# Kernel optimization log

Hardware: AMD Instinct MI355X
Metric: run time of the kernel (lower is better)

The kernel has to match this reference:

```python
import jax, jax.numpy as jnp
import numpy as np

D_MODEL, D_FF, N_EXPERTS, TOP_K = 1024, 4096, 8, 2
B, S = 4, 2048


def setup_inputs() -> dict:
    key = jax.random.key(0)
    ks = jax.random.split(key, 6)
    scale_in = 1.0 / np.sqrt(D_MODEL)
    scale_ff = 1.0 / np.sqrt(D_FF)
    return {
        "x": jax.random.normal(ks[0], (B, S, D_MODEL), jnp.float32),
        "gate_w": jax.random.normal(ks[1], (N_EXPERTS, D_MODEL), jnp.float32) * 0.01,
        "w1": jax.random.normal(ks[2], (N_EXPERTS, D_MODEL, D_FF), jnp.float32) * scale_in,
        "b1": jax.random.normal(ks[3], (N_EXPERTS, D_FF), jnp.float32) * 0.01,
        "w2": jax.random.normal(ks[4], (N_EXPERTS, D_FF, D_MODEL), jnp.float32) * scale_ff,
        "b2": jax.random.normal(ks[5], (N_EXPERTS, D_MODEL), jnp.float32) * 0.01,
    }


def reference(x, gate_w, w1, b1, w2, b2):
    # x: [B, S, D]; gate_w: [E, D]; w1: [E, D, F]; w2: [E, F, D]
    Bb, Ss, D = x.shape
    E = gate_w.shape[0]
    logits = jnp.einsum("bsd,ed->bse", x, gate_w)
    probs = jax.nn.softmax(logits, axis=-1)
    top_p, top_i = jax.lax.top_k(probs, TOP_K)                # [B,S,K]
    top_p = top_p / (jnp.sum(top_p, axis=-1, keepdims=True) + 1e-9)
    T = Bb * Ss
    x_flat = x.reshape(T, D)
    idx = top_i.reshape(T, TOP_K)
    val = top_p.reshape(T, TOP_K)
    # per-token combine weight for each expert: [T, E]
    comb = jnp.zeros((T, E), x.dtype).at[jnp.arange(T)[:, None], idx].add(val)
    out = jnp.zeros_like(x_flat)
    for e in range(E):  # small fixed expert count
        h = jax.nn.gelu(x_flat @ w1[e] + b1[e], approximate=False)
        y = h @ w2[e] + b2[e]
        out = out + y * comb[:, e:e + 1]
    return out.reshape(Bb, Ss, D)
```

## Files before the change

kernel.cpp:

```cpp
#include <hip/hip_runtime.h>
#include <hip/hip_bf16.h>
#include <cstdint>

#define D_MODEL 1024
#define D_FF    4096
#define NEXP    8
#define TOPK    2
#define TOKENS  8192
#define NPAIR   (TOKENS * TOPK)
#define NPAD    (NPAIR + 128)

typedef __bf16 bf16x8 __attribute__((ext_vector_type(8)));
typedef float  f32x4  __attribute__((ext_vector_type(4)));

__device__ __forceinline__ unsigned short f2bf(float f) {
    unsigned int u = __float_as_uint(f);
    unsigned int r = (u + 0x7FFFu + ((u >> 16) & 1u)) >> 16;
    return (unsigned short)r;
}

__device__ __forceinline__ void lds_load16(void* lds, const void* g) {
    __builtin_amdgcn_global_load_lds(
        (const __attribute__((address_space(1))) void*)g,
        (__attribute__((address_space(3))) void*)lds, 16, 0, 0);
}

__device__ __forceinline__ float fast_gelu(float v) {
    float y2 = 1.5957691216f * (v + 0.044715f * v * v * v);
    float t = 1.0f - 2.0f / (__expf(y2) + 1.0f);
    return 0.5f * v * (1.0f + t);
}

__global__ __launch_bounds__(64) void gate_kernel(
        const float* __restrict__ x, const float* __restrict__ gw,
        int* __restrict__ tok_e, float* __restrict__ tok_w)
{
    const int t = blockIdx.x;
    const int lane = threadIdx.x;
    const float* xr = x + (size_t)t * D_MODEL;
    float xv[16];
#pragma unroll
    for (int i = 0; i < 16; ++i) xv[i] = xr[lane + 64 * i];
    float lg[NEXP];
#pragma unroll
    for (int e = 0; e < NEXP; ++e) {
        const float* g = gw + e * D_MODEL;
        float s = 0.f;
#pragma unroll
        for (int i = 0; i < 16; ++i) s += xv[i] * g[lane + 64 * i];
        for (int off = 32; off; off >>= 1) s += __shfl_down(s, off);
        lg[e] = s;
    }
    if (lane == 0) {
        float m = lg[0];
#pragma unroll
        for (int e = 1; e < NEXP; ++e) m = fmaxf(m, lg[e]);
        float ex[NEXP], S = 0.f;
#pragma unroll
        for (int e = 0; e < NEXP; ++e) { ex[e] = expf(lg[e] - m); S += ex[e]; }
        int i0 = 0; float p0 = ex[0];
#pragma unroll
        for (int e = 1; e < NEXP; ++e) if (ex[e] > p0) { p0 = ex[e]; i0 = e; }
        int i1 = -1; float p1 = -1.f;
#pragma unroll
        for (int e = 0; e < NEXP; ++e) if (e != i0 && ex[e] > p1) { p1 = ex[e]; i1 = e; }
        float q0 = p0 / S, q1 = p1 / S;
        float denom = q0 + q1 + 1e-9f;
        tok_e[2 * t] = i0; tok_e[2 * t + 1] = i1;
        tok_w[2 * t] = q0 / denom; tok_w[2 * t + 1] = q1 / denom;
    }
}

__global__ __launch_bounds__(256) void count_kernel(
        const int* __restrict__ tok_e, int* __restrict__ cnt)
{
    __shared__ int lc[NEXP];
    const int t = blockIdx.x * 256 + threadIdx.x;
    if (threadIdx.x < NEXP) lc[threadIdx.x] = 0;
    __syncthreads();
    atomicAdd(&lc[tok_e[2 * t]], 1);
    atomicAdd(&lc[tok_e[2 * t + 1]], 1);
    __syncthreads();
    if (threadIdx.x < NEXP) atomicAdd(&cnt[threadIdx.x], lc[threadIdx.x]);
}

__global__ void offsets_kernel(const int* __restrict__ cnt, int* __restrict__ offs,
                               int* __restrict__ fill)
{
    if (threadIdx.x == 0 && blockIdx.x == 0) {
        int s = 0;
        for (int e = 0; e < NEXP; ++e) { offs[e] = s; fill[e] = s; s += cnt[e]; }
        offs[NEXP] = s;
    }
}

__global__ __launch_bounds__(256) void scatter2_kernel(
        const int* __restrict__ tok_e, const float* __restrict__ tok_w,
        int* __restrict__ fill, int* __restrict__ pair_tok, float* __restrict__ pair_w)
{
    __shared__ int lc[NEXP], lbase[NEXP];
    const int t = blockIdx.x * 256 + threadIdx.x;
    if (threadIdx.x < NEXP) lc[threadIdx.x] = 0;
    __syncthreads();
    const int e0 = tok_e[2 * t], e1 = tok_e[2 * t + 1];
    const int r0 = atomicAdd(&lc[e0], 1);
    const int r1 = atomicAdd(&lc[e1], 1);
    __syncthreads();
    if (threadIdx.x < NEXP)
        lbase[threadIdx.x] = atomicAdd(&fill[threadIdx.x], lc[threadIdx.x]);
    __syncthreads();
    const int p0 = lbase[e0] + r0, p1 = lbase[e1] + r1;
    pair_tok[p0] = t; pair_w[p0] = tok_w[2 * t];
    pair_tok[p1] = t; pair_w[p1] = tok_w[2 * t + 1];
}

__global__ __launch_bounds__(256) void gather_cvt(
        const float* __restrict__ x, const int* __restrict__ pair_tok,
        unsigned short* __restrict__ Xg)
{
    int p = blockIdx.x;
    int tok = pair_tok[p];
    const float4* src = (const float4*)(x + (size_t)tok * D_MODEL);
    ushort4* dst = (ushort4*)(Xg + (size_t)p * D_MODEL);
    float4 v = src[threadIdx.x];
    ushort4 o;
    o.x = f2bf(v.x); o.y = f2bf(v.y); o.z = f2bf(v.z); o.w = f2bf(v.w);
    dst[threadIdx.x] = o;
}

__global__ __launch_bounds__(256) void transpose_cvt(
        const float* __restrict__ in, unsigned short* __restrict__ out, int R, int C)
{
    __shared__ float tile[32][33];
    const int e = blockIdx.z;
    const int r0 = blockIdx.y * 32, c0 = blockIdx.x * 32;
    const float* src = in + (size_t)e * R * C;
    unsigned short* dst = out + (size_t)e * R * C;
    const int tx = threadIdx.x & 31, ty = threadIdx.x >> 5;
#pragma unroll
    for (int i = 0; i < 32; i += 8)
        tile[ty + i][tx] = src[(size_t)(r0 + ty + i) * C + (c0 + tx)];
    __syncthreads();
#pragma unroll
    for (int i = 0; i < 32; i += 8)
        dst[(size_t)(c0 + ty + i) * R + (r0 + tx)] = f2bf(tile[tx][ty + i]);
}

#define MOE_STAGE3(PA, PB, K0, LD) \
    lds_load16(PA + t * 8,        ag + (K0)); \
    lds_load16(PA + 2048 + t * 8, ag + (size_t)64 * (LD) + (K0)); \
    lds_load16(PB + t * 8,        bg + (K0)); \
    lds_load16(PB + 2048 + t * 8, bg + (size_t)64 * (LD) + (K0));

#define MOE_COMPUTE3(PA, PB) { \
    bf16x8 a_[4], b_[4]; \
    _Pragma("unroll") \
    for (int i_ = 0; i_ < 4; ++i_) { \
        a_[i_] = *(const bf16x8*)&PA[(wm * 64 + i_ * 16 + lm) * 32 + qs8]; \
        b_[i_] = *(const bf16x8*)&PB[(wn * 64 + i_ * 16 + lm) * 32 + qs8]; \
    } \
    __builtin_amdgcn_s_setprio(1); \
    _Pragma("unroll") \
    for (int i_ = 0; i_ < 4; ++i_) \
    _Pragma("unroll") \
    for (int j_ = 0; j_ < 4; ++j_) \
        c[i_][j_] = __builtin_amdgcn_mfma_f32_16x16x32_bf16(a_[i_], b_[j_], c[i_][j_], 0, 0, 0); \
    __builtin_amdgcn_s_setprio(0); }

#define MOE_KLOOP(KTOT, LD) \
    MOE_STAGE3(sa0, sb0, 0, LD) \
    MOE_STAGE3(sa1, sb1, 32, LD) \
    for (int kt = 0; kt < (KTOT) - 64; kt += 32) { \
        MOE_STAGE3(sa2, sb2, kt + 64, LD) \
        asm volatile("s_waitcnt vmcnt(8)" ::: "memory"); \
        __builtin_amdgcn_s_barrier(); \
        MOE_COMPUTE3(sa0, sb0) \
        __builtin_amdgcn_s_barrier(); \
        unsigned short* tA_ = sa0; sa0 = sa1; sa1 = sa2; sa2 = tA_; \
        unsigned short* tB_ = sb0; sb0 = sb1; sb1 = sb2; sb2 = tB_; \
    } \
    asm volatile("s_waitcnt vmcnt(4)" ::: "memory"); \
    __builtin_amdgcn_s_barrier(); \
    MOE_COMPUTE3(sa0, sb0) \
    asm volatile("s_waitcnt vmcnt(0)" ::: "memory"); \
    __builtin_amdgcn_s_barrier(); \
    MOE_COMPUTE3(sa1, sb1)

#define MOE_SWIZZLE(XT, YT) \
    { int d_ = blockIdx.y * gridDim.x + blockIdx.x; \
      int xcd_ = d_ & 7, k_ = d_ >> 3; \
      XT = k_ % gridDim.x; \
      YT = (k_ / gridDim.x) * 8 + xcd_; }

__global__ __launch_bounds__(256, 3) void gemm1_kernel(
        const unsigned short* __restrict__ Xg, const unsigned short* __restrict__ w1t,
        const float* __restrict__ b1, const int* __restrict__ offs,
        unsigned short* __restrict__ H)
{
    int xt, yt;
    MOE_SWIZZLE(xt, yt)
    const int e = blockIdx.z;
    const int seg1 = offs[e + 1];
    const int row0 = offs[e] + yt * 128;
    if (row0 >= seg1) return;
    const int n0 = xt * 128;

    __shared__ __align__(16) unsigned short SA[3 * 128 * 32];
    __shared__ __align__(16) unsigned short SB[3 * 128 * 32];
    unsigned short *sa0 = SA, *sa1 = SA + 4096, *sa2 = SA + 8192;
    unsigned short *sb0 = SB, *sb1 = SB + 4096, *sb2 = SB + 8192;

    const int t = threadIdx.x;
    const int ca = (((t & 3) ^ ((t >> 3) & 3))) * 8;
    const unsigned short* ag = Xg + (size_t)(row0 + (t >> 2)) * D_MODEL + ca;
    const unsigned short* bg = w1t + (size_t)e * D_FF * D_MODEL
                                   + (size_t)(n0 + (t >> 2)) * D_MODEL + ca;

    const int wave = t >> 6, lane = t & 63;
    const int wm = wave & 1, wn = wave >> 1;
    const int lm = lane & 15, quad = lane >> 4;
    const int qs8 = (quad ^ ((lm >> 1) & 3)) * 8;

    f32x4 c[4][4] = {};

    MOE_KLOOP(D_MODEL, D_MODEL)

    float bb[4];
#pragma unroll
    for (int j = 0; j < 4; ++j)
        bb[j] = b1[e * D_FF + n0 + wn * 64 + j * 16 + lm];
#pragma unroll
    for (int i = 0; i < 4; ++i) {
#pragma unroll
        for (int r = 0; r < 4; ++r) {
            int gm = row0 + wm * 64 + i * 16 + quad * 4 + r;
            if (gm < seg1) {
#pragma unroll
                for (int j = 0; j < 4; ++j) {
                    int gn = n0 + wn * 64 + j * 16 + lm;
                    float v = c[i][j][r] + bb[j];
                    H[(size_t)gm * D_FF + gn] = f2bf(fast_gelu(v));
                }
            }
        }
    }
}

__global__ __launch_bounds__(256, 3) void gemm2_kernel(
        const unsigned short* __restrict__ H, const unsigned short* __restrict__ w2t,
        const float* __restrict__ b2, const int* __restrict__ offs,
        const int* __restrict__ pair_tok, const float* __restrict__ pair_w,
        float* __restrict__ out)
{
    int xt, yt;
    MOE_SWIZZLE(xt, yt)
    const int e = blockIdx.z;
    const int seg1 = offs[e + 1];
    const int row0 = offs[e] + yt * 128;
    if (row0 >= seg1) return;
    const int n0 = xt * 128;

    __shared__ __align__(16) unsigned short SA[3 * 128 * 32];
    __shared__ __align__(16) unsigned short SB[3 * 128 * 32];
    unsigned short *sa0 = SA, *sa1 = SA + 4096, *sa2 = SA + 8192;
    unsigned short *sb0 = SB, *sb1 = SB + 4096, *sb2 = SB + 8192;

    const int t = threadIdx.x;
    const int ca = (((t & 3) ^ ((t >> 3) & 3))) * 8;
    const unsigned short* ag = H + (size_t)(row0 + (t >> 2)) * D_FF + ca;
    const unsigned short* bg = w2t + (size_t)e * D_MODEL * D_FF
                                   + (size_t)(n0 + (t >> 2)) * D_FF + ca;

    const int wave = t >> 6, lane = t & 63;
    const int wm = wave & 1, wn = wave >> 1;
    const int lm = lane & 15, quad = lane >> 4;
    const int qs8 = (quad ^ ((lm >> 1) & 3)) * 8;

    f32x4 c[4][4] = {};

    MOE_KLOOP(D_FF, D_FF)

    float bb[4];
#pragma unroll
    for (int j = 0; j < 4; ++j)
        bb[j] = b2[e * D_MODEL + n0 + wn * 64 + j * 16 + lm];
#pragma unroll
    for (int i = 0; i < 4; ++i) {
#pragma unroll
        for (int r = 0; r < 4; ++r) {
            int gm = row0 + wm * 64 + i * 16 + quad * 4 + r;
            if (gm < seg1) {
                int tok = pair_tok[gm];
                float wgt = pair_w[gm];
#pragma unroll
                for (int j = 0; j < 4; ++j) {
                    int gn = n0 + wn * 64 + j * 16 + lm;
                    float v = (c[i][j][r] + bb[j]) * wgt;
                    atomicAdd(&out[(size_t)tok * D_MODEL + gn], v);
                }
            }
        }
    }
}

extern "C" void kernel_launch(void* const* d_in, const int* in_sizes, int n_in,
                              void* d_out, int out_size, void* d_ws, size_t ws_size,
                              hipStream_t stream)
{
    const float* x      = (const float*)d_in[0];
    const float* gate_w = (const float*)d_in[1];
    const float* w1     = (const float*)d_in[2];
    const float* b1     = (const float*)d_in[3];
    const float* w2     = (const float*)d_in[4];
    const float* b2     = (const float*)d_in[5];
    float* out = (float*)d_out;

    char* ws = (char*)d_ws;
    const size_t WT_OFF   = 0;
    const size_t XG_OFF   = WT_OFF + (size_t)NEXP * D_FF * D_MODEL * 2;
    const size_t H_OFF    = XG_OFF + (size_t)NPAD * D_MODEL * 2;
    const size_t PTOK_OFF = H_OFF + (size_t)NPAD * D_FF * 2;
    const size_t PW_OFF   = PTOK_OFF + (size_t)NPAD * 4;
    const size_t TOKE_OFF = PW_OFF + (size_t)NPAD * 4;
    const size_t TOKW_OFF = TOKE_OFF + (size_t)NPAIR * 4;
    const size_t CNT_OFF  = TOKW_OFF + (size_t)NPAIR * 4;

    unsigned short* wt  = (unsigned short*)(ws + WT_OFF);
    unsigned short* Xg  = (unsigned short*)(ws + XG_OFF);
    unsigned short* H   = (unsigned short*)(ws + H_OFF);
    int*   pair_tok = (int*)(ws + PTOK_OFF);
    float* pair_w   = (float*)(ws + PW_OFF);
    int*   tok_e    = (int*)(ws + TOKE_OFF);
    float* tok_w    = (float*)(ws + TOKW_OFF);
    int*   cnt      = (int*)(ws + CNT_OFF);
    int*   fill     = cnt + 8;
    int*   offs     = cnt + 16;

    (void)hipMemsetAsync(cnt, 0, 64, stream);
    (void)hipMemsetAsync(out, 0, (size_t)out_size * sizeof(float), stream);

    gate_kernel<<<TOKENS, 64, 0, stream>>>(x, gate_w, tok_e, tok_w);
    count_kernel<<<TOKENS / 256, 256, 0, stream>>>(tok_e, cnt);
    offsets_kernel<<<1, 64, 0, stream>>>(cnt, offs, fill);
    scatter2_kernel<<<TOKENS / 256, 256, 0, stream>>>(tok_e, tok_w, fill, pair_tok, pair_w);
    gather_cvt<<<NPAIR, 256, 0, stream>>>(x, pair_tok, Xg);

    transpose_cvt<<<dim3(D_FF / 32, D_MODEL / 32, NEXP), 256, 0, stream>>>(w1, wt, D_MODEL, D_FF);
    gemm1_kernel<<<dim3(D_FF / 128, TOKENS / 128, NEXP), 256, 0, stream>>>(Xg, wt, b1, offs, H);
    transpose_cvt<<<dim3(D_MODEL / 32, D_FF / 32, NEXP), 256, 0, stream>>>(w2, wt, D_FF, D_MODEL);
    gemm2_kernel<<<dim3(D_MODEL / 128, TOKENS / 128, NEXP), 256, 0, stream>>>(H, wt, b2, offs, pair_tok, pair_w, out);
}
```

Before: 833.3 us.

## Enlarge MoE GEMM tiles to 256x128 with 8 waves and LDS-staged H stores

Both expert GEMMs now use 512-thread blocks, each covering 256 token rows by 128 columns. Each B tile loaded into LDS is reused across twice as many rows, which cuts weight traffic per FLOP; the wait counts are adjusted for three loads per stage. The gemm1 epilogue now writes GELU results into a swizzled LDS buffer in two halves and stores them to H as coalesced 16-byte chunks, replacing scattered 2-byte stores. In exchange, LDS use per block and padding waste at expert segment ends both grow, which may lower occupancy.

New measurement: 888.1 us. 1.07x slower.

```diff
diff --git a/kernel.cpp b/kernel.cpp
--- a/kernel.cpp
+++ b/kernel.cpp
@@ -8,7 +8,7 @@
 #define TOPK    2
 #define TOKENS  8192
 #define NPAIR   (TOKENS * TOPK)
-#define NPAD    (NPAIR + 128)
+#define NPAD    (NPAIR + 256)
 
 typedef __bf16 bf16x8 __attribute__((ext_vector_type(8)));
 typedef float  f32x4  __attribute__((ext_vector_type(4)));
@@ -148,9 +148,8 @@
 
 #define MOE_STAGE3(PA, PB, K0, LD) \
     lds_load16(PA + t * 8,        ag + (K0)); \
-    lds_load16(PA + 2048 + t * 8, ag + (size_t)64 * (LD) + (K0)); \
-    lds_load16(PB + t * 8,        bg + (K0)); \
-    lds_load16(PB + 2048 + t * 8, bg + (size_t)64 * (LD) + (K0));
+    lds_load16(PA + 4096 + t * 8, ag + (size_t)128 * (LD) + (K0)); \
+    lds_load16(PB + t * 8,        bg + (K0));
 
 #define MOE_COMPUTE3(PA, PB) { \
     bf16x8 a_[4], b_[4]; \
@@ -172,14 +171,14 @@
     MOE_STAGE3(sa1, sb1, 32, LD) \
     for (int kt = 0; kt < (KTOT) - 64; kt += 32) { \
         MOE_STAGE3(sa2, sb2, kt + 64, LD) \
-        asm volatile("s_waitcnt vmcnt(8)" ::: "memory"); \
+        asm volatile("s_waitcnt vmcnt(6)" ::: "memory"); \
         __builtin_amdgcn_s_barrier(); \
         MOE_COMPUTE3(sa0, sb0) \
         __builtin_amdgcn_s_barrier(); \
         unsigned short* tA_ = sa0; sa0 = sa1; sa1 = sa2; sa2 = tA_; \
         unsigned short* tB_ = sb0; sb0 = sb1; sb1 = sb2; sb2 = tB_; \
     } \
-    asm volatile("s_waitcnt vmcnt(4)" ::: "memory"); \
+    asm volatile("s_waitcnt vmcnt(3)" ::: "memory"); \
     __builtin_amdgcn_s_barrier(); \
     MOE_COMPUTE3(sa0, sb0) \
     asm volatile("s_waitcnt vmcnt(0)" ::: "memory"); \
@@ -192,7 +191,7 @@
       XT = k_ % gridDim.x; \
       YT = (k_ / gridDim.x) * 8 + xcd_; }
 
-__global__ __launch_bounds__(256, 3) void gemm1_kernel(
+__global__ __launch_bounds__(512, 4) void gemm1_kernel(
         const unsigned short* __restrict__ Xg, const unsigned short* __restrict__ w1t,
         const float* __restrict__ b1, const int* __restrict__ offs,
         unsigned short* __restrict__ H)
@@ -201,13 +200,13 @@
     MOE_SWIZZLE(xt, yt)
     const int e = blockIdx.z;
     const int seg1 = offs[e + 1];
-    const int row0 = offs[e] + yt * 128;
+    const int row0 = offs[e] + yt * 256;
     if (row0 >= seg1) return;
     const int n0 = xt * 128;
 
-    __shared__ __align__(16) unsigned short SA[3 * 128 * 32];
+    __shared__ __align__(16) unsigned short SA[3 * 256 * 32];
     __shared__ __align__(16) unsigned short SB[3 * 128 * 32];
-    unsigned short *sa0 = SA, *sa1 = SA + 4096, *sa2 = SA + 8192;
+    unsigned short *sa0 = SA, *sa1 = SA + 8192, *sa2 = SA + 16384;
     unsigned short *sb0 = SB, *sb1 = SB + 4096, *sb2 = SB + 8192;
 
     const int t = threadIdx.x;
@@ -217,7 +216,7 @@
                                    + (size_t)(n0 + (t >> 2)) * D_MODEL + ca;
 
     const int wave = t >> 6, lane = t & 63;
-    const int wm = wave & 1, wn = wave >> 1;
+    const int wm = wave >> 1, wn = wave & 1;
     const int lm = lane & 15, quad = lane >> 4;
     const int qs8 = (quad ^ ((lm >> 1) & 3)) * 8;
 
@@ -229,24 +228,43 @@
 #pragma unroll
     for (int j = 0; j < 4; ++j)
         bb[j] = b1[e * D_FF + n0 + wn * 64 + j * 16 + lm];
-#pragma unroll
-    for (int i = 0; i < 4; ++i) {
-#pragma unroll
-        for (int r = 0; r < 4; ++r) {
-            int gm = row0 + wm * 64 + i * 16 + quad * 4 + r;
-            if (gm < seg1) {
+
+    const int myp = wm >> 1;
+    const int rb = (wm & 1) * 64;
+    __syncthreads();
+#pragma unroll
+    for (int p = 0; p < 2; ++p) {
+        if (myp == p) {
+#pragma unroll
+            for (int i = 0; i < 4; ++i)
+#pragma unroll
+            for (int r = 0; r < 4; ++r) {
+                int rl = rb + i * 16 + quad * 4 + r;
 #pragma unroll
                 for (int j = 0; j < 4; ++j) {
-                    int gn = n0 + wn * 64 + j * 16 + lm;
+                    int col = wn * 64 + j * 16 + lm;
                     float v = c[i][j][r] + bb[j];
-                    H[(size_t)gm * D_FF + gn] = f2bf(fast_gelu(v));
+                    SA[rl * 128 + (((col >> 3) ^ (rl & 7)) << 3) + (col & 7)] =
+                        f2bf(fast_gelu(v));
                 }
             }
         }
-    }
-}
-
-__global__ __launch_bounds__(256, 3) void gemm2_kernel(
+        __syncthreads();
+#pragma unroll
+        for (int it = 0; it < 4; ++it) {
+            int g = it * 512 + t;
+            int rl = g >> 4, cch = g & 15;
+            int grow = row0 + p * 128 + rl;
+            if (grow < seg1) {
+                uint4 vv = *(const uint4*)&SA[rl * 128 + ((cch ^ (rl & 7)) << 3)];
+                *(uint4*)(H + (size_t)grow * D_FF + n0 + cch * 8) = vv;
+            }
+        }
+        __syncthreads();
+    }
+}
+
+__global__ __launch_bounds__(512, 4) void gemm2_kernel(
         const unsigned short* __restrict__ H, const unsigned short* __restrict__ w2t,
         const float* __restrict__ b2, const int* __restrict__ offs,
         const int* __restrict__ pair_tok, const float* __restrict__ pair_w,
@@ -256,13 +274,13 @@
     MOE_SWIZZLE(xt, yt)
     const int e = blockIdx.z;
     const int seg1 = offs[e + 1];
-    const int row0 = offs[e] + yt * 128;
+    const int row0 = offs[e] + yt * 256;
     if (row0 >= seg1) return;
     const int n0 = xt * 128;
 
-    __shared__ __align__(16) unsigned short SA[3 * 128 * 32];
+    __shared__ __align__(16) unsigned short SA[3 * 256 * 32];
     __shared__ __align__(16) unsigned short SB[3 * 128 * 32];
-    unsigned short *sa0 = SA, *sa1 = SA + 4096, *sa2 = SA + 8192;
+    unsigned short *sa0 = SA, *sa1 = SA + 8192, *sa2 = SA + 16384;
     unsigned short *sb0 = SB, *sb1 = SB + 4096, *sb2 = SB + 8192;
 
     const int t = threadIdx.x;
@@ -272,7 +290,7 @@
                                    + (size_t)(n0 + (t >> 2)) * D_FF + ca;
 
     const int wave = t >> 6, lane = t & 63;
-    const int wm = wave & 1, wn = wave >> 1;
+    const int wm = wave >> 1, wn = wave & 1;
     const int lm = lane & 15, quad = lane >> 4;
     const int qs8 = (quad ^ ((lm >> 1) & 3)) * 8;
 
@@ -346,7 +364,7 @@
     gather_cvt<<<NPAIR, 256, 0, stream>>>(x, pair_tok, Xg);
 
     transpose_cvt<<<dim3(D_FF / 32, D_MODEL / 32, NEXP), 256, 0, stream>>>(w1, wt, D_MODEL, D_FF);
-    gemm1_kernel<<<dim3(D_FF / 128, TOKENS / 128, NEXP), 256, 0, stream>>>(Xg, wt, b1, offs, H);
+    gemm1_kernel<<<dim3(D_FF / 128, NPAIR / 256, NEXP), 512, 0, stream>>>(Xg, wt, b1, offs, H);
     transpose_cvt<<<dim3(D_MODEL / 32, D_FF / 32, NEXP), 256, 0, stream>>>(w2, wt, D_FF, D_MODEL);
-    gemm2_kernel<<<dim3(D_MODEL / 128, TOKENS / 128, NEXP), 256, 0, stream>>>(H, wt, b2, offs, pair_tok, pair_w, out);
-}
+    gemm2_kernel<<<dim3(D_MODEL / 128, NPAIR / 256, NEXP), 512, 0, stream>>>(H, wt, b2, offs, pair_tok, pair_w, out);
+}
```
